# Kernel optimization log

Measured on AMD Instinct MI355X. Metric: run time of the kernel, lower is better.

The kernel has to match this reference:

```python
import jax, jax.numpy as jnp
import numpy as np

N = 4096      # Hadamard size (power of 2, = hidden dim)
ROWS = 8192   # tokens being rotated (batch*seq)


def _hadamard_matrix(n: int) -> np.ndarray:
    """Sylvester Hadamard matrix H[i,j] = (-1)^popcount(i & j), scaled by 1/sqrt(n)."""
    idx = np.arange(n, dtype=np.int64)
    m = idx[:, None] & idx[None, :]
    pop = np.zeros_like(m)
    for _ in range(int(np.log2(n))):
        pop += m & 1
        m >>= 1
    H = np.where(pop % 2 == 0, 1.0, -1.0).astype(np.float32)
    return H / np.sqrt(np.float32(n))


def setup_inputs() -> dict:
    key = jax.random.key(0)
    k_val, = jax.random.split(key, 1)
    value = jax.random.normal(k_val, (ROWS, N), dtype=jnp.float32)
    weight = jnp.asarray(_hadamard_matrix(N))
    # one-hot permutation matrix (deterministic)
    rng = np.random.RandomState(0)
    perm = rng.permutation(N)
    P = np.zeros((N, N), dtype=np.float32)
    P[np.arange(N), perm] = 1.0
    permutation = jnp.asarray(P)
    return {"value": value, "weight": weight, "permutation": permutation}


def reference(value, weight, permutation):
    # forward: transform_weight = weight + permutation; side='right' ->
    # rotated value = value @ transform_weight
    w = weight + permutation              # [N, N]
    return jnp.matmul(value, w)           # [ROWS, N]
```

## Files before the change

kernel.cpp:

```cpp
#include <hip/hip_runtime.h>

#define HN 4096
#define HROWS 8192

__global__ void extract_inv_kernel(const float4* __restrict__ P4,
                                   int* __restrict__ inv) {
    const int total = (HN * HN) / 4;
    const int stride = gridDim.x * blockDim.x;
    for (int i = blockIdx.x * blockDim.x + threadIdx.x; i < total; i += stride) {
        float4 p = P4[i];
        if (p.x != 0.0f || p.y != 0.0f || p.z != 0.0f || p.w != 0.0f) {
            int base = i << 2;
            int row = base >> 12;
            int col = base & (HN - 1);
            if (p.x != 0.0f) inv[col]     = row;
            if (p.y != 0.0f) inv[col + 1] = row;
            if (p.z != 0.0f) inv[col + 2] = row;
            if (p.w != 0.0f) inv[col + 3] = row;
        }
    }
}

__device__ __forceinline__ void fwht16(float* x) {
#pragma unroll
    for (int s = 1; s < 16; s <<= 1) {
#pragma unroll
        for (int i = 0; i < 16; ++i) {
            if ((i & s) == 0) {
                float u = x[i], w = x[i + s];
                x[i] = u + w;
                x[i + s] = u - w;
            }
        }
    }
}

#define WORK_SZ 5248
#define ORIG_SZ 4608

__global__ __launch_bounds__(256, 4)
void fwht_perm_kernel(const float* __restrict__ val,
                      const int* __restrict__ inv,
                      float* __restrict__ out) {
    __shared__ __align__(16) float work[WORK_SZ];
    __shared__ __align__(16) float orig[ORIG_SZ];

    const int t = threadIdx.x;
    const int row = blockIdx.x;
    const float* vr = val + (size_t)row * HN;
    float* outr = out + (size_t)row * HN;

    float x[16];

    const float4* vr4 = (const float4*)vr + (t << 2);
    float4 a0 = vr4[0], a1 = vr4[1], a2 = vr4[2], a3 = vr4[3];

    float4* o4 = (float4*)(orig + (t << 4) + ((t >> 1) << 2));
    o4[0] = a0; o4[1] = a1; o4[2] = a2; o4[3] = a3;

    x[0] = a0.x; x[1] = a0.y; x[2]  = a0.z; x[3]  = a0.w;
    x[4] = a1.x; x[5] = a1.y; x[6]  = a1.z; x[7]  = a1.w;
    x[8] = a2.x; x[9] = a2.y; x[10] = a2.z; x[11] = a2.w;
    x[12] = a3.x; x[13] = a3.y; x[14] = a3.z; x[15] = a3.w;

    fwht16(x);

    float4* w4 = (float4*)(work + 20 * t + ((t >> 4) << 3));
    w4[0] = make_float4(x[0],  x[1],  x[2],  x[3]);
    w4[1] = make_float4(x[4],  x[5],  x[6],  x[7]);
    w4[2] = make_float4(x[8],  x[9],  x[10], x[11]);
    w4[3] = make_float4(x[12], x[13], x[14], x[15]);
    __syncthreads();

    const int hi = t >> 4;
    const int lo = t & 15;

    {
        const int base = 328 * hi + lo;
#pragma unroll
        for (int m = 0; m < 16; ++m) x[m] = work[base + 20 * m];
        fwht16(x);
#pragma unroll
        for (int m = 0; m < 16; ++m) work[base + 20 * m] = x[m];
    }
    __syncthreads();

    {
        const int base = 20 * hi + lo;
#pragma unroll
        for (int m = 0; m < 16; ++m) x[m] = work[base + 328 * m];
        fwht16(x);
    }

    const int j0 = (hi << 4) | lo;
#pragma unroll
    for (int m = 0; m < 16; ++m) {
        int j = (m << 8) + j0;
        int src = inv[j];
        int so = src + ((src >> 5) << 2);
        outr[j] = x[m] * 0.015625f + orig[so];
    }
}

extern "C" void kernel_launch(void* const* d_in, const int* in_sizes, int n_in,
                              void* d_out, int out_size, void* d_ws, size_t ws_size,
                              hipStream_t stream) {
    const float* value = (const float*)d_in[0];
    const float* permutation = (const float*)d_in[2];
    float* out = (float*)d_out;
    int* inv = (int*)d_ws;

    extract_inv_kernel<<<2048, 256, 0, stream>>>((const float4*)permutation, inv);
    fwht_perm_kernel<<<HROWS, 256, 0, stream>>>(value, inv, out);
}
```

Measured before the change: 293.1 us.

## Reuse one shared buffer for gather and FWHT, coalesce loads, raise occupancy

New measurement: 293.2 us. No clear change (+0.0%).

```diff
diff --git a/kernel.cpp b/kernel.cpp
--- a/kernel.cpp
+++ b/kernel.cpp
@@ -35,70 +35,79 @@
     }
 }
 
-#define WORK_SZ 5248
-#define ORIG_SZ 4608
+#define WORK_SZ 4352
 
-__global__ __launch_bounds__(256, 4)
+__global__ __launch_bounds__(256, 6)
 void fwht_perm_kernel(const float* __restrict__ val,
                       const int* __restrict__ inv,
                       float* __restrict__ out) {
     __shared__ __align__(16) float work[WORK_SZ];
-    __shared__ __align__(16) float orig[ORIG_SZ];
 
     const int t = threadIdx.x;
-    const int row = blockIdx.x;
-    const float* vr = val + (size_t)row * HN;
-    float* outr = out + (size_t)row * HN;
+    const float* vr = val + (size_t)blockIdx.x * HN;
+    float* outr = out + (size_t)blockIdx.x * HN;
+
+    const int c2 = t & 63;
+    const int m2 = t >> 6;
+
+    int gslot[16];
+#pragma unroll
+    for (int u = 0; u < 16; ++u) {
+        int iv = inv[c2 + (u << 6) + (m2 << 10)];
+        gslot[u] = iv + ((iv >> 6) << 2);
+    }
+
+    const float4* vr4 = (const float4*)vr;
+    float4 a0 = vr4[t];
+    float4 a1 = vr4[t + 256];
+    float4 a2 = vr4[t + 512];
+    float4 a3 = vr4[t + 768];
+
+#define W4PTR(q) ((float4*)(work + ((((q) + ((q) >> 4))) << 2)))
+    *W4PTR(t)       = a0;
+    *W4PTR(t + 256) = a1;
+    *W4PTR(t + 512) = a2;
+    *W4PTR(t + 768) = a3;
+    __syncthreads();
+
+    float g[16];
+#pragma unroll
+    for (int u = 0; u < 16; ++u) g[u] = work[gslot[u]];
 
     float x[16];
-
-    const float4* vr4 = (const float4*)vr + (t << 2);
-    float4 a0 = vr4[0], a1 = vr4[1], a2 = vr4[2], a3 = vr4[3];
-
-    float4* o4 = (float4*)(orig + (t << 4) + ((t >> 1) << 2));
-    o4[0] = a0; o4[1] = a1; o4[2] = a2; o4[3] = a3;
-
-    x[0] = a0.x; x[1] = a0.y; x[2]  = a0.z; x[3]  = a0.w;
-    x[4] = a1.x; x[5] = a1.y; x[6]  = a1.z; x[7]  = a1.w;
-    x[8] = a2.x; x[9] = a2.y; x[10] = a2.z; x[11] = a2.w;
+    x[0]  = a0.x; x[1]  = a0.y; x[2]  = a0.z; x[3]  = a0.w;
+    x[4]  = a1.x; x[5]  = a1.y; x[6]  = a1.z; x[7]  = a1.w;
+    x[8]  = a2.x; x[9]  = a2.y; x[10] = a2.z; x[11] = a2.w;
     x[12] = a3.x; x[13] = a3.y; x[14] = a3.z; x[15] = a3.w;
-
     fwht16(x);
-
-    float4* w4 = (float4*)(work + 20 * t + ((t >> 4) << 3));
-    w4[0] = make_float4(x[0],  x[1],  x[2],  x[3]);
-    w4[1] = make_float4(x[4],  x[5],  x[6],  x[7]);
-    w4[2] = make_float4(x[8],  x[9],  x[10], x[11]);
-    w4[3] = make_float4(x[12], x[13], x[14], x[15]);
     __syncthreads();
 
-    const int hi = t >> 4;
-    const int lo = t & 15;
+    *W4PTR(t)       = make_float4(x[0],  x[1],  x[2],  x[3]);
+    *W4PTR(t + 256) = make_float4(x[4],  x[5],  x[6],  x[7]);
+    *W4PTR(t + 512) = make_float4(x[8],  x[9],  x[10], x[11]);
+    *W4PTR(t + 768) = make_float4(x[12], x[13], x[14], x[15]);
+    __syncthreads();
 
     {
-        const int base = 328 * hi + lo;
+        const int base = (t & 3) + 68 * (t >> 2);
 #pragma unroll
-        for (int m = 0; m < 16; ++m) x[m] = work[base + 20 * m];
+        for (int u = 0; u < 16; ++u) x[u] = work[base + (u << 2)];
         fwht16(x);
 #pragma unroll
-        for (int m = 0; m < 16; ++m) work[base + 20 * m] = x[m];
+        for (int u = 0; u < 16; ++u) work[base + (u << 2)] = x[u];
     }
     __syncthreads();
 
     {
-        const int base = 20 * hi + lo;
+        const int base = c2 + 1088 * m2;
 #pragma unroll
-        for (int m = 0; m < 16; ++m) x[m] = work[base + 328 * m];
+        for (int u = 0; u < 16; ++u) x[u] = work[base + 68 * u];
         fwht16(x);
     }
 
-    const int j0 = (hi << 4) | lo;
 #pragma unroll
-    for (int m = 0; m < 16; ++m) {
-        int j = (m << 8) + j0;
-        int src = inv[j];
-        int so = src + ((src >> 5) << 2);
-        outr[j] = x[m] * 0.015625f + orig[so];
+    for (int u = 0; u < 16; ++u) {
+        outr[c2 + (u << 6) + (m2 << 10)] = x[u] * 0.015625f + g[u];
     }
 }
 
@@ -110,6 +119,6 @@
     float* out = (float*)d_out;
     int* inv = (int*)d_ws;
 
-    extract_inv_kernel<<<2048, 256, 0, stream>>>((const float4*)permutation, inv);
+    extract_inv_kernel<<<4096, 256, 0, stream>>>((const float4*)permutation, inv);
     fwht_perm_kernel<<<HROWS, 256, 0, stream>>>(value, inv, out);
 }
```
